# Kernel tuning notes

Hardware: AMD Instinct MI355X
Metric: run time of the kernel (lower is better)

Reference implementation:

```python
import jax, jax.numpy as jnp
import numpy as np

N = 100000  # nodes
NEG_SLOPE = 0.2


def gat_conv(x, W, att_src, att_dst, bias, src, dst):
    # x: [N, Fin], W: [Fin, Fout], att_*: [Fout], bias: [Fout]
    h = x @ W                                    # [N, Fout]
    a_s = h @ att_src                            # [N]
    a_d = h @ att_dst                            # [N]
    e = jax.nn.leaky_relu(a_s[src] + a_d[dst], NEG_SLOPE)  # [E]
    # segment softmax over destination-node neighborhoods
    m = jax.ops.segment_max(e, dst, num_segments=N)        # [N]
    ex = jnp.exp(e - m[dst])
    denom = jax.ops.segment_sum(ex, dst, num_segments=N)   # [N]
    alpha = ex / denom[dst]                      # [E]
    out = jax.ops.segment_sum(alpha[:, None] * h[src], dst, num_segments=N)
    return out + bias


def setup_inputs() -> dict:
    key = jax.random.key(0)
    ks = jax.random.split(key, 10)
    F_in, H, C, E = 512, 16, 40, 3200000
    x = jax.random.normal(ks[0], (N, F_in), dtype=jnp.float32)
    edge_index = jax.random.randint(ks[1], (2, E), 0, N, dtype=jnp.int64)
    s1 = 1.0 / np.sqrt(F_in)
    s2 = 1.0 / np.sqrt(H)
    return {
        "x": x,
        "W1": jax.random.normal(ks[2], (F_in, H), dtype=jnp.float32) * s1,
        "att_src1": jax.random.normal(ks[3], (H,), dtype=jnp.float32) * s2,
        "att_dst1": jax.random.normal(ks[4], (H,), dtype=jnp.float32) * s2,
        "bias1": jnp.zeros((H,), dtype=jnp.float32),
        "W2": jax.random.normal(ks[5], (H, C), dtype=jnp.float32) * s2,
        "att_src2": jax.random.normal(ks[6], (C,), dtype=jnp.float32) / np.sqrt(C),
        "att_dst2": jax.random.normal(ks[7], (C,), dtype=jnp.float32) / np.sqrt(C),
        "bias2": jnp.zeros((C,), dtype=jnp.float32),
        "edge_index": edge_index,
    }


def reference(x, W1, att_src1, att_dst1, bias1, W2, att_src2, att_dst2, bias2, edge_index):
    # add self loops (PyG GATConv default add_self_loops=True)
    loop = jnp.arange(N, dtype=edge_index.dtype)
    src = jnp.concatenate([edge_index[0], loop])
    dst = jnp.concatenate([edge_index[1], loop])
    h = gat_conv(x, W1, att_src1, att_dst1, bias1, src, dst)
    h = jax.nn.relu(h)  # dropout is identity in eval mode
    out = gat_conv(h, W2, att_src2, att_dst2, bias2, src, dst)
    return out
```

## Files before the change

### kernel.cpp

```cpp
#include <hip/hip_runtime.h>
#include <math.h>


constexpr int FIN = 512;
constexpr int F1  = 16;
constexpr int C2  = 40;
constexpr float SLOPE = 0.2f;
constexpr int BSH   = 8;
constexpr int NBMAX = 512;
constexpr int LDSE  = 9728;

__global__ __launch_bounds__(128) void k1_gemm(
    const float* __restrict__ x, const float* __restrict__ W1,
    const float* __restrict__ att_s, const float* __restrict__ att_d,
    float* __restrict__ h1, float* __restrict__ a_s, float* __restrict__ a_d, int n)
{
    __shared__ float WT[F1][FIN + 4];
    for (int idx = threadIdx.x; idx < FIN * F1; idx += 128) {
        int k = idx >> 4, o = idx & 15;
        WT[o][k] = W1[idx];
    }
    __syncthreads();

    const int o0 = (threadIdx.x & 3) * 4;
    const int ng = threadIdx.x >> 2;
    const int node0 = blockIdx.x * 128 + ng * 4;

    const float* xr[4];
#pragma unroll
    for (int nn = 0; nn < 4; ++nn) {
        int node = node0 + nn;
        xr[nn] = x + (size_t)(node < n ? node : 0) * FIN;
    }

    float acc[4][4] = {};
    for (int k = 0; k < FIN; k += 4) {
        float4 wv[4];
#pragma unroll
        for (int oo = 0; oo < 4; ++oo) wv[oo] = *(const float4*)&WT[o0 + oo][k];
#pragma unroll
        for (int nn = 0; nn < 4; ++nn) {
            float4 xv = *(const float4*)(xr[nn] + k);
#pragma unroll
            for (int oo = 0; oo < 4; ++oo)
                acc[nn][oo] += xv.x * wv[oo].x + xv.y * wv[oo].y +
                               xv.z * wv[oo].z + xv.w * wv[oo].w;
        }
    }

#pragma unroll
    for (int nn = 0; nn < 4; ++nn) {
        int node = node0 + nn;
        float ps = 0.f, pd = 0.f;
#pragma unroll
        for (int oo = 0; oo < 4; ++oo) {
            ps += acc[nn][oo] * att_s[o0 + oo];
            pd += acc[nn][oo] * att_d[o0 + oo];
        }
        ps += __shfl_xor(ps, 1); ps += __shfl_xor(ps, 2);
        pd += __shfl_xor(pd, 1); pd += __shfl_xor(pd, 2);
        if (node < n) {
            *(float4*)&h1[(size_t)node * F1 + o0] =
                make_float4(acc[nn][0], acc[nn][1], acc[nn][2], acc[nn][3]);
            if ((threadIdx.x & 3) == 0) { a_s[node] = ps; a_d[node] = pd; }
        }
    }
}

__global__ __launch_bounds__(256) void k_bhist(const int* __restrict__ dst,
                                               int* __restrict__ bcnt, int E, int nb)
{
    __shared__ int cnt[NBMAX];
    for (int t = threadIdx.x; t < NBMAX; t += 256) cnt[t] = 0;
    __syncthreads();
    int base = blockIdx.x * 4096;
#pragma unroll
    for (int k = 0; k < 16; ++k) {
        int e = base + k * 256 + threadIdx.x;
        if (e < E) atomicAdd(&cnt[dst[e] >> BSH], 1);
    }
    __syncthreads();
    for (int t = threadIdx.x; t < nb; t += 256) {
        int c = cnt[t];
        if (c) atomicAdd(&bcnt[t], c);
    }
}

__global__ __launch_bounds__(512) void k_bscan(const int* __restrict__ bcnt,
                                               int* __restrict__ bbase,
                                               int* __restrict__ gcur, int nb, int E)
{
    __shared__ int sc[512];
    int t = threadIdx.x;
    int v = (t < nb) ? bcnt[t] : 0;
    sc[t] = v; __syncthreads();
    for (int off = 1; off < 512; off <<= 1) {
        int u = (t >= off) ? sc[t - off] : 0;
        __syncthreads();
        sc[t] += u;
        __syncthreads();
    }
    int excl = sc[t] - v;
    if (t < nb) { bbase[t] = excl; gcur[t] = excl; }
    if (t == 0) bbase[nb] = E;
}

__global__ __launch_bounds__(256) void k_bucket(const int* __restrict__ src,
                                                const int* __restrict__ dst,
                                                int* __restrict__ gcur,
                                                unsigned int* __restrict__ bpk, int E)
{
    __shared__ int cnt[NBMAX];
    __shared__ int cur[NBMAX];
    for (int t = threadIdx.x; t < NBMAX; t += 256) cnt[t] = 0;
    __syncthreads();
    int base = blockIdx.x * 4096;
#pragma unroll
    for (int k = 0; k < 16; ++k) {
        int e = base + k * 256 + threadIdx.x;
        if (e < E) atomicAdd(&cnt[dst[e] >> BSH], 1);
    }
    __syncthreads();
    for (int t = threadIdx.x; t < NBMAX; t += 256) {
        int c = cnt[t];
        cur[t] = c ? atomicAdd(&gcur[t], c) : 0;
    }
    __syncthreads();
#pragma unroll
    for (int k = 0; k < 16; ++k) {
        int e = base + k * 256 + threadIdx.x;
        if (e < E) {
            int d = dst[e];
            int b = d >> BSH;
            int pos = atomicAdd(&cur[b], 1);
            bpk[pos] = (unsigned)src[e] | ((unsigned)(d & ((1 << BSH) - 1)) << 17);
        }
    }
}

__global__ __launch_bounds__(256) void f1_agg(
    const unsigned int* __restrict__ bpk, const int* __restrict__ bbase,
    const float* __restrict__ h1, const float* __restrict__ a_s, const float* __restrict__ a_d,
    const float* __restrict__ bias1, const float* __restrict__ W2,
    const float* __restrict__ att_s2, const float* __restrict__ att_d2,
    float* __restrict__ hin2, float* __restrict__ pa_s, float* __restrict__ pa_d, int n)
{
    __shared__ int lsrc[LDSE];
    __shared__ int cnt[256];
    __shared__ int scn[256];
    __shared__ float vs[F1], vd[F1], bl[F1];
    const int b = blockIdx.x, t = threadIdx.x;
    const int beg = bbase[b], end = bbase[b + 1];
    const int m = end - beg;

    if (t < 32) {
        int f = t & 15;
        const float* att = (t < 16) ? att_s2 : att_d2;
        float sum = 0.f;
        for (int c = 0; c < C2; ++c) sum += W2[f * C2 + c] * att[c];
        if (t < 16) vs[f] = sum; else vd[f] = sum;
    } else if (t < 48) {
        bl[t - 32] = bias1[t - 32];
    }
    cnt[t] = 0;
    __syncthreads();

    int myBeg = 0, myCnt = 0;
    const bool fits = (m <= LDSE);
    if (fits) {
        for (int j = beg + t; j < end; j += 256)
            atomicAdd(&cnt[(bpk[j] >> 17) & 255], 1);
        __syncthreads();
        int v = cnt[t];
        scn[t] = v;
        __syncthreads();
        for (int off = 1; off < 256; off <<= 1) {
            int u = (t >= off) ? scn[t - off] : 0;
            __syncthreads();
            scn[t] += u;
            __syncthreads();
        }
        myCnt = v;
        myBeg = scn[t] - v;
        cnt[t] = myBeg;
        __syncthreads();
        for (int j = beg + t; j < end; j += 256) {
            unsigned pk = bpk[j];
            int p = atomicAdd(&cnt[(pk >> 17) & 255], 1);
            lsrc[p] = (int)(pk & 0x1FFFFu);
        }
        __syncthreads();
    }

    const int node = (b << BSH) + t;
    if (node >= n) return;

    const float adi = a_d[node];
    float acc[F1];
#pragma unroll
    for (int f = 0; f < F1; ++f) acc[f] = 0.f;
    float den = 0.f;

    if (fits) {
        for (int k = 0; k < myCnt; ++k) {
            int s = lsrc[myBeg + k];
            float ev = a_s[s] + adi;
            ev = (ev >= 0.f) ? ev : SLOPE * ev;
            float ex = __expf(ev);
            den += ex;
            const float4* hp = (const float4*)(h1 + (size_t)s * F1);
#pragma unroll
            for (int q = 0; q < 4; ++q) {
                float4 v = hp[q];
                acc[4*q+0] += ex * v.x; acc[4*q+1] += ex * v.y;
                acc[4*q+2] += ex * v.z; acc[4*q+3] += ex * v.w;
            }
        }
    } else {
        for (int j = beg; j < end; ++j) {
            unsigned pk = bpk[j];
            if ((int)((pk >> 17) & 255) != t) continue;
            int s = (int)(pk & 0x1FFFFu);
            float ev = a_s[s] + adi;
            ev = (ev >= 0.f) ? ev : SLOPE * ev;
            float ex = __expf(ev);
            den += ex;
            const float4* hp = (const float4*)(h1 + (size_t)s * F1);
#pragma unroll
            for (int q = 0; q < 4; ++q) {
                float4 v = hp[q];
                acc[4*q+0] += ex * v.x; acc[4*q+1] += ex * v.y;
                acc[4*q+2] += ex * v.z; acc[4*q+3] += ex * v.w;
            }
        }
    }

    float evs = a_s[node] + adi;
    evs = (evs >= 0.f) ? evs : SLOPE * evs;
    float exs = __expf(evs);
    const float4* hs = (const float4*)(h1 + (size_t)node * F1);
    float inv;
    {
        float d2 = den + exs;
        inv = 1.f / d2;
    }
    float ps = 0.f, pd = 0.f;
    float4* ho = (float4*)(hin2 + (size_t)node * F1);
#pragma unroll
    for (int q = 0; q < 4; ++q) {
        float4 sv = hs[q];
        float4 V;
        V.x = fmaxf((acc[4*q+0] + exs * sv.x) * inv + bl[4*q+0], 0.f);
        V.y = fmaxf((acc[4*q+1] + exs * sv.y) * inv + bl[4*q+1], 0.f);
        V.z = fmaxf((acc[4*q+2] + exs * sv.z) * inv + bl[4*q+2], 0.f);
        V.w = fmaxf((acc[4*q+3] + exs * sv.w) * inv + bl[4*q+3], 0.f);
        ho[q] = V;
        ps += V.x * vs[4*q+0] + V.y * vs[4*q+1] + V.z * vs[4*q+2] + V.w * vs[4*q+3];
        pd += V.x * vd[4*q+0] + V.y * vd[4*q+1] + V.z * vd[4*q+2] + V.w * vd[4*q+3];
    }
    pa_s[node] = ps; pa_d[node] = pd;
}

__global__ __launch_bounds__(256) void f2_agg(
    const unsigned int* __restrict__ bpk, const int* __restrict__ bbase,
    const float* __restrict__ hin2, const float* __restrict__ a_s, const float* __restrict__ a_d,
    const float* __restrict__ W2, const float* __restrict__ bias2,
    float* __restrict__ out, int n)
{
    __shared__ int lsrc[LDSE];
    __shared__ int cnt[256];
    __shared__ int scn[256];
    __shared__ float W2s[F1 * C2];
    __shared__ float b2[C2];
    const int b = blockIdx.x, t = threadIdx.x;
    const int beg = bbase[b], end = bbase[b + 1];
    const int m = end - beg;

    for (int idx = t; idx < F1 * C2; idx += 256) W2s[idx] = W2[idx];
    if (t < C2) b2[t] = bias2[t];
    cnt[t] = 0;
    __syncthreads();

    int myBeg = 0, myCnt = 0;
    const bool fits = (m <= LDSE);
    if (fits) {
        for (int j = beg + t; j < end; j += 256)
            atomicAdd(&cnt[(bpk[j] >> 17) & 255], 1);
        __syncthreads();
        int v = cnt[t];
        scn[t] = v;
        __syncthreads();
        for (int off = 1; off < 256; off <<= 1) {
            int u = (t >= off) ? scn[t - off] : 0;
            __syncthreads();
            scn[t] += u;
            __syncthreads();
        }
        myCnt = v;
        myBeg = scn[t] - v;
        cnt[t] = myBeg;
        __syncthreads();
        for (int j = beg + t; j < end; j += 256) {
            unsigned pk = bpk[j];
            int p = atomicAdd(&cnt[(pk >> 17) & 255], 1);
            lsrc[p] = (int)(pk & 0x1FFFFu);
        }
        __syncthreads();
    }

    const int node = (b << BSH) + t;
    if (node >= n) return;

    const float adi = a_d[node];
    float acc[F1];
#pragma unroll
    for (int f = 0; f < F1; ++f) acc[f] = 0.f;
    float den = 0.f;

    if (fits) {
        for (int k = 0; k < myCnt; ++k) {
            int s = lsrc[myBeg + k];
            float ev = a_s[s] + adi;
            ev = (ev >= 0.f) ? ev : SLOPE * ev;
            float ex = __expf(ev);
            den += ex;
            const float4* hp = (const float4*)(hin2 + (size_t)s * F1);
#pragma unroll
            for (int q = 0; q < 4; ++q) {
                float4 v = hp[q];
                acc[4*q+0] += ex * v.x; acc[4*q+1] += ex * v.y;
                acc[4*q+2] += ex * v.z; acc[4*q+3] += ex * v.w;
            }
        }
    } else {
        for (int j = beg; j < end; ++j) {
            unsigned pk = bpk[j];
            if ((int)((pk >> 17) & 255) != t) continue;
            int s = (int)(pk & 0x1FFFFu);
            float ev = a_s[s] + adi;
            ev = (ev >= 0.f) ? ev : SLOPE * ev;
            float ex = __expf(ev);
            den += ex;
            const float4* hp = (const float4*)(hin2 + (size_t)s * F1);
#pragma unroll
            for (int q = 0; q < 4; ++q) {
                float4 v = hp[q];
                acc[4*q+0] += ex * v.x; acc[4*q+1] += ex * v.y;
                acc[4*q+2] += ex * v.z; acc[4*q+3] += ex * v.w;
            }
        }
    }

    float evs = a_s[node] + adi;
    evs = (evs >= 0.f) ? evs : SLOPE * evs;
    float exs = __expf(evs);
    const float4* hs = (const float4*)(hin2 + (size_t)node * F1);
    float inv = 1.f / (den + exs);
    float val[F1];
#pragma unroll
    for (int q = 0; q < 4; ++q) {
        float4 sv = hs[q];
        val[4*q+0] = (acc[4*q+0] + exs * sv.x) * inv;
        val[4*q+1] = (acc[4*q+1] + exs * sv.y) * inv;
        val[4*q+2] = (acc[4*q+2] + exs * sv.z) * inv;
        val[4*q+3] = (acc[4*q+3] + exs * sv.w) * inv;
    }
    float* op = out + (size_t)node * C2;
    for (int c0 = 0; c0 < C2; c0 += 4) {
        float4 r = make_float4(b2[c0], b2[c0+1], b2[c0+2], b2[c0+3]);
#pragma unroll
        for (int f = 0; f < F1; ++f) {
            float v = val[f];
            r.x += v * W2s[f * C2 + c0 + 0];
            r.y += v * W2s[f * C2 + c0 + 1];
            r.z += v * W2s[f * C2 + c0 + 2];
            r.w += v * W2s[f * C2 + c0 + 3];
        }
        *(float4*)(op + c0) = r;
    }
}

extern "C" void kernel_launch(void* const* d_in, const int* in_sizes, int n_in,
                              void* d_out, int out_size, void* d_ws, size_t ws_size,
                              hipStream_t stream) {
    const float* x      = (const float*)d_in[0];
    const float* W1     = (const float*)d_in[1];
    const float* att_s1 = (const float*)d_in[2];
    const float* att_d1 = (const float*)d_in[3];
    const float* bias1  = (const float*)d_in[4];
    const float* W2     = (const float*)d_in[5];
    const float* att_s2 = (const float*)d_in[6];
    const float* att_d2 = (const float*)d_in[7];
    const float* bias2  = (const float*)d_in[8];
    const int*   edge   = (const int*)d_in[9];

    const int n = in_sizes[0] / FIN;
    const int E = in_sizes[9] / 2;
    const int* src = edge;
    const int* dst = edge + E;
    const int NBK = (n + (1 << BSH) - 1) >> BSH;

    size_t Ns = (size_t)n;
    float* h1    = (float*)d_ws;
    float* hin2  = h1   + 16 * Ns;
    float* a_s1  = hin2 + 16 * Ns;
    float* a_d1  = a_s1 + Ns;
    float* pa_s2 = a_d1 + Ns;
    float* pa_d2 = pa_s2 + Ns;
    int*   bcnt  = (int*)(pa_d2 + Ns);
    int*   bbase = bcnt + NBMAX;
    int*   gcur  = bbase + NBMAX + 1;
    unsigned int* bpk = (unsigned int*)(gcur + NBMAX);
    float* out   = (float*)d_out;

    const int gbA = (E + 4095) / 4096;
    const int gb1 = (n + 127) / 128;

    hipMemsetAsync(bcnt, 0, sizeof(int) * NBMAX, stream);
    k_bhist <<<gbA, 256, 0, stream>>>(dst, bcnt, E, NBK);
    k_bscan <<<1, 512, 0, stream>>>(bcnt, bbase, gcur, NBK, E);
    k_bucket<<<gbA, 256, 0, stream>>>(src, dst, gcur, bpk, E);
    k1_gemm <<<gb1, 128, 0, stream>>>(x, W1, att_s1, att_d1, h1, a_s1, a_d1, n);
    f1_agg  <<<NBK, 256, 0, stream>>>(bpk, bbase, h1, a_s1, a_d1, bias1, W2,
                                      att_s2, att_d2, hin2, pa_s2, pa_d2, n);
    f2_agg  <<<NBK, 256, 0, stream>>>(bpk, bbase, hin2, pa_s2, pa_d2, W2, bias2, out, n);
}
```

Measured before the change: 587.4 us.

## Split aggregation buckets into sub-blocks with four threads per node

Each 256-node destination bucket is now handled by four blocks, each owning 64 nodes, and each node's 16 features are split across four threads that each own one float4. This raises parallelism and occupancy in the aggregation kernels, shrinks per-block LDS to a 3072-entry sub-bucket, and swaps the barrier-heavy 256-wide scan for a 64-lane shuffle scan. The second-layer output projection now goes through shared memory so that four threads share it. The GEMM block size is also doubled to 256. Each sub-block still scans the whole bucket's packed edge list, so bucket reads are repeated four times.

```diff
diff --git a/kernel.cpp b/kernel.cpp
--- a/kernel.cpp
+++ b/kernel.cpp
@@ -8,15 +8,15 @@
 constexpr float SLOPE = 0.2f;
 constexpr int BSH   = 8;
 constexpr int NBMAX = 512;
-constexpr int LDSE  = 9728;
-
-__global__ __launch_bounds__(128) void k1_gemm(
+constexpr int SUBE  = 3072;
+
+__global__ __launch_bounds__(256) void k1_gemm(
     const float* __restrict__ x, const float* __restrict__ W1,
     const float* __restrict__ att_s, const float* __restrict__ att_d,
     float* __restrict__ h1, float* __restrict__ a_s, float* __restrict__ a_d, int n)
 {
     __shared__ float WT[F1][FIN + 4];
-    for (int idx = threadIdx.x; idx < FIN * F1; idx += 128) {
+    for (int idx = threadIdx.x; idx < FIN * F1; idx += 256) {
         int k = idx >> 4, o = idx & 15;
         WT[o][k] = W1[idx];
     }
@@ -24,7 +24,7 @@
 
     const int o0 = (threadIdx.x & 3) * 4;
     const int ng = threadIdx.x >> 2;
-    const int node0 = blockIdx.x * 128 + ng * 4;
+    const int node0 = blockIdx.x * 256 + ng * 4;
 
     const float* xr[4];
 #pragma unroll
@@ -145,13 +145,12 @@
     const float* __restrict__ att_s2, const float* __restrict__ att_d2,
     float* __restrict__ hin2, float* __restrict__ pa_s, float* __restrict__ pa_d, int n)
 {
-    __shared__ int lsrc[LDSE];
-    __shared__ int cnt[256];
-    __shared__ int scn[256];
+    __shared__ int lsrc[SUBE];
+    __shared__ int cnt[64], cur[64], sbeg[64];
     __shared__ float vs[F1], vd[F1], bl[F1];
-    const int b = blockIdx.x, t = threadIdx.x;
+    const int t = threadIdx.x;
+    const int b = blockIdx.x >> 2, sb = blockIdx.x & 3;
     const int beg = bbase[b], end = bbase[b + 1];
-    const int m = end - beg;
 
     if (t < 32) {
         int f = t & 15;
@@ -162,103 +161,90 @@
     } else if (t < 48) {
         bl[t - 32] = bias1[t - 32];
     }
-    cnt[t] = 0;
-    __syncthreads();
-
-    int myBeg = 0, myCnt = 0;
-    const bool fits = (m <= LDSE);
+    if (t < 64) cnt[t] = 0;
+    __syncthreads();
+
+    for (int j = beg + t; j < end; j += 256) {
+        unsigned pk = bpk[j];
+        if (((pk >> 23) & 3u) == (unsigned)sb)
+            atomicAdd(&cnt[(pk >> 17) & 63], 1);
+    }
+    __syncthreads();
+    if (t < 64) {
+        int v = cnt[t], s = v;
+#pragma unroll
+        for (int off = 1; off < 64; off <<= 1) {
+            int u = __shfl_up(s, off);
+            if (t >= off) s += u;
+        }
+        sbeg[t] = s - v;
+        cur[t]  = s - v;
+    }
+    __syncthreads();
+    const int msub = sbeg[63] + cnt[63];
+    const bool fits = (msub <= SUBE);
     if (fits) {
-        for (int j = beg + t; j < end; j += 256)
-            atomicAdd(&cnt[(bpk[j] >> 17) & 255], 1);
-        __syncthreads();
-        int v = cnt[t];
-        scn[t] = v;
-        __syncthreads();
-        for (int off = 1; off < 256; off <<= 1) {
-            int u = (t >= off) ? scn[t - off] : 0;
-            __syncthreads();
-            scn[t] += u;
-            __syncthreads();
-        }
-        myCnt = v;
-        myBeg = scn[t] - v;
-        cnt[t] = myBeg;
-        __syncthreads();
         for (int j = beg + t; j < end; j += 256) {
             unsigned pk = bpk[j];
-            int p = atomicAdd(&cnt[(pk >> 17) & 255], 1);
-            lsrc[p] = (int)(pk & 0x1FFFFu);
-        }
-        __syncthreads();
-    }
-
-    const int node = (b << BSH) + t;
+            if (((pk >> 23) & 3u) == (unsigned)sb) {
+                int p = atomicAdd(&cur[(pk >> 17) & 63], 1);
+                lsrc[p] = (int)(pk & 0x1FFFFu);
+            }
+        }
+    }
+    __syncthreads();
+
+    const int nl = t >> 2, sub = t & 3;
+    const int node = (b << BSH) + (sb << 6) + nl;
     if (node >= n) return;
 
     const float adi = a_d[node];
-    float acc[F1];
-#pragma unroll
-    for (int f = 0; f < F1; ++f) acc[f] = 0.f;
-    float den = 0.f;
+    float a0 = 0.f, a1 = 0.f, a2 = 0.f, a3 = 0.f, den = 0.f;
 
     if (fits) {
-        for (int k = 0; k < myCnt; ++k) {
-            int s = lsrc[myBeg + k];
+        const int mb = sbeg[nl], mc = cnt[nl];
+        const float* hq = h1 + 4 * sub;
+        for (int k = 0; k < mc; ++k) {
+            int s = lsrc[mb + k];
             float ev = a_s[s] + adi;
             ev = (ev >= 0.f) ? ev : SLOPE * ev;
             float ex = __expf(ev);
             den += ex;
-            const float4* hp = (const float4*)(h1 + (size_t)s * F1);
-#pragma unroll
-            for (int q = 0; q < 4; ++q) {
-                float4 v = hp[q];
-                acc[4*q+0] += ex * v.x; acc[4*q+1] += ex * v.y;
-                acc[4*q+2] += ex * v.z; acc[4*q+3] += ex * v.w;
-            }
+            float4 v = *(const float4*)(hq + (size_t)s * F1);
+            a0 += ex * v.x; a1 += ex * v.y; a2 += ex * v.z; a3 += ex * v.w;
         }
     } else {
+        const unsigned key = ((unsigned)sb << 6) | (unsigned)nl;
+        const float* hq = h1 + 4 * sub;
         for (int j = beg; j < end; ++j) {
             unsigned pk = bpk[j];
-            if ((int)((pk >> 17) & 255) != t) continue;
+            if (((pk >> 17) & 255u) != key) continue;
             int s = (int)(pk & 0x1FFFFu);
             float ev = a_s[s] + adi;
             ev = (ev >= 0.f) ? ev : SLOPE * ev;
             float ex = __expf(ev);
             den += ex;
-            const float4* hp = (const float4*)(h1 + (size_t)s * F1);
-#pragma unroll
-            for (int q = 0; q < 4; ++q) {
-                float4 v = hp[q];
-                acc[4*q+0] += ex * v.x; acc[4*q+1] += ex * v.y;
-                acc[4*q+2] += ex * v.z; acc[4*q+3] += ex * v.w;
-            }
+            float4 v = *(const float4*)(hq + (size_t)s * F1);
+            a0 += ex * v.x; a1 += ex * v.y; a2 += ex * v.z; a3 += ex * v.w;
         }
     }
 
     float evs = a_s[node] + adi;
     evs = (evs >= 0.f) ? evs : SLOPE * evs;
     float exs = __expf(evs);
-    const float4* hs = (const float4*)(h1 + (size_t)node * F1);
-    float inv;
-    {
-        float d2 = den + exs;
-        inv = 1.f / d2;
-    }
-    float ps = 0.f, pd = 0.f;
-    float4* ho = (float4*)(hin2 + (size_t)node * F1);
-#pragma unroll
-    for (int q = 0; q < 4; ++q) {
-        float4 sv = hs[q];
-        float4 V;
-        V.x = fmaxf((acc[4*q+0] + exs * sv.x) * inv + bl[4*q+0], 0.f);
-        V.y = fmaxf((acc[4*q+1] + exs * sv.y) * inv + bl[4*q+1], 0.f);
-        V.z = fmaxf((acc[4*q+2] + exs * sv.z) * inv + bl[4*q+2], 0.f);
-        V.w = fmaxf((acc[4*q+3] + exs * sv.w) * inv + bl[4*q+3], 0.f);
-        ho[q] = V;
-        ps += V.x * vs[4*q+0] + V.y * vs[4*q+1] + V.z * vs[4*q+2] + V.w * vs[4*q+3];
-        pd += V.x * vd[4*q+0] + V.y * vd[4*q+1] + V.z * vd[4*q+2] + V.w * vd[4*q+3];
-    }
-    pa_s[node] = ps; pa_d[node] = pd;
+    float inv = 1.f / (den + exs);
+    float4 sv = *(const float4*)(h1 + (size_t)node * F1 + 4 * sub);
+    float4 V;
+    V.x = fmaxf((a0 + exs * sv.x) * inv + bl[4*sub+0], 0.f);
+    V.y = fmaxf((a1 + exs * sv.y) * inv + bl[4*sub+1], 0.f);
+    V.z = fmaxf((a2 + exs * sv.z) * inv + bl[4*sub+2], 0.f);
+    V.w = fmaxf((a3 + exs * sv.w) * inv + bl[4*sub+3], 0.f);
+    *(float4*)(hin2 + (size_t)node * F1 + 4 * sub) = V;
+    float ps = V.x * vs[4*sub+0] + V.y * vs[4*sub+1] + V.z * vs[4*sub+2] + V.w * vs[4*sub+3];
+    float pd = V.x * vd[4*sub+0] + V.y * vd[4*sub+1] + V.z * vd[4*sub+2] + V.w * vd[4*sub+3];
+    ps += __shfl_xor(ps, 1, 4); ps += __shfl_xor(ps, 2, 4);
+    pd += __shfl_xor(pd, 1, 4); pd += __shfl_xor(pd, 2, 4);
+    if (sub == 0) { pa_s[node] = ps; pa_d[node] = pd; }
 }
 
 __global__ __launch_bounds__(256) void f2_agg(
@@ -267,116 +253,102 @@
     const float* __restrict__ W2, const float* __restrict__ bias2,
     float* __restrict__ out, int n)
 {
-    __shared__ int lsrc[LDSE];
-    __shared__ int cnt[256];
-    __shared__ int scn[256];
+    __shared__ int lsrc[SUBE];
+    __shared__ int cnt[64], cur[64], sbeg[64];
     __shared__ float W2s[F1 * C2];
     __shared__ float b2[C2];
-    const int b = blockIdx.x, t = threadIdx.x;
+    __shared__ float vals[64][F1 + 1];
+    const int t = threadIdx.x;
+    const int b = blockIdx.x >> 2, sb = blockIdx.x & 3;
     const int beg = bbase[b], end = bbase[b + 1];
-    const int m = end - beg;
 
     for (int idx = t; idx < F1 * C2; idx += 256) W2s[idx] = W2[idx];
     if (t < C2) b2[t] = bias2[t];
-    cnt[t] = 0;
-    __syncthreads();
-
-    int myBeg = 0, myCnt = 0;
-    const bool fits = (m <= LDSE);
+    if (t < 64) cnt[t] = 0;
+    __syncthreads();
+
+    for (int j = beg + t; j < end; j += 256) {
+        unsigned pk = bpk[j];
+        if (((pk >> 23) & 3u) == (unsigned)sb)
+            atomicAdd(&cnt[(pk >> 17) & 63], 1);
+    }
+    __syncthreads();
+    if (t < 64) {
+        int v = cnt[t], s = v;
+#pragma unroll
+        for (int off = 1; off < 64; off <<= 1) {
+            int u = __shfl_up(s, off);
+            if (t >= off) s += u;
+        }
+        sbeg[t] = s - v;
+        cur[t]  = s - v;
+    }
+    __syncthreads();
+    const int msub = sbeg[63] + cnt[63];
+    const bool fits = (msub <= SUBE);
     if (fits) {
-        for (int j = beg + t; j < end; j += 256)
-            atomicAdd(&cnt[(bpk[j] >> 17) & 255], 1);
-        __syncthreads();
-        int v = cnt[t];
-        scn[t] = v;
-        __syncthreads();
-        for (int off = 1; off < 256; off <<= 1) {
-            int u = (t >= off) ? scn[t - off] : 0;
-            __syncthreads();
-            scn[t] += u;
-            __syncthreads();
-        }
-        myCnt = v;
-        myBeg = scn[t] - v;
-        cnt[t] = myBeg;
-        __syncthreads();
         for (int j = beg + t; j < end; j += 256) {
             unsigned pk = bpk[j];
-            int p = atomicAdd(&cnt[(pk >> 17) & 255], 1);
-            lsrc[p] = (int)(pk & 0x1FFFFu);
-        }
-        __syncthreads();
-    }
-
-    const int node = (b << BSH) + t;
+            if (((pk >> 23) & 3u) == (unsigned)sb) {
+                int p = atomicAdd(&cur[(pk >> 17) & 63], 1);
+                lsrc[p] = (int)(pk & 0x1FFFFu);
+            }
+        }
+    }
+    __syncthreads();
+
+    const int nl = t >> 2, sub = t & 3;
+    const int node = (b << BSH) + (sb << 6) + nl;
     if (node >= n) return;
 
     const float adi = a_d[node];
-    float acc[F1];
-#pragma unroll
-    for (int f = 0; f < F1; ++f) acc[f] = 0.f;
-    float den = 0.f;
+    float a0 = 0.f, a1 = 0.f, a2 = 0.f, a3 = 0.f, den = 0.f;
 
     if (fits) {
-        for (int k = 0; k < myCnt; ++k) {
-            int s = lsrc[myBeg + k];
+        const int mb = sbeg[nl], mc = cnt[nl];
+        const float* hq = hin2 + 4 * sub;
+        for (int k = 0; k < mc; ++k) {
+            int s = lsrc[mb + k];
             float ev = a_s[s] + adi;
             ev = (ev >= 0.f) ? ev : SLOPE * ev;
             float ex = __expf(ev);
             den += ex;
-            const float4* hp = (const float4*)(hin2 + (size_t)s * F1);
-#pragma unroll
-            for (int q = 0; q < 4; ++q) {
-                float4 v = hp[q];
-                acc[4*q+0] += ex * v.x; acc[4*q+1] += ex * v.y;
-                acc[4*q+2] += ex * v.z; acc[4*q+3] += ex * v.w;
-            }
+            float4 v = *(const float4*)(hq + (size_t)s * F1);
+            a0 += ex * v.x; a1 += ex * v.y; a2 += ex * v.z; a3 += ex * v.w;
         }
     } else {
+        const unsigned key = ((unsigned)sb << 6) | (unsigned)nl;
+        const float* hq = hin2 + 4 * sub;
         for (int j = beg; j < end; ++j) {
             unsigned pk = bpk[j];
-            if ((int)((pk >> 17) & 255) != t) continue;
+            if (((pk >> 17) & 255u) != key) continue;
             int s = (int)(pk & 0x1FFFFu);
             float ev = a_s[s] + adi;
             ev = (ev >= 0.f) ? ev : SLOPE * ev;
             float ex = __expf(ev);
             den += ex;
-            const float4* hp = (const float4*)(hin2 + (size_t)s * F1);
-#pragma unroll
-            for (int q = 0; q < 4; ++q) {
-                float4 v = hp[q];
-                acc[4*q+0] += ex * v.x; acc[4*q+1] += ex * v.y;
-                acc[4*q+2] += ex * v.z; acc[4*q+3] += ex * v.w;
-            }
+            float4 v = *(const float4*)(hq + (size_t)s * F1);
+            a0 += ex * v.x; a1 += ex * v.y; a2 += ex * v.z; a3 += ex * v.w;
         }
     }
 
     float evs = a_s[node] + adi;
     evs = (evs >= 0.f) ? evs : SLOPE * evs;
     float exs = __expf(evs);
-    const float4* hs = (const float4*)(hin2 + (size_t)node * F1);
     float inv = 1.f / (den + exs);
-    float val[F1];
-#pragma unroll
-    for (int q = 0; q < 4; ++q) {
-        float4 sv = hs[q];
-        val[4*q+0] = (acc[4*q+0] + exs * sv.x) * inv;
-        val[4*q+1] = (acc[4*q+1] + exs * sv.y) * inv;
-        val[4*q+2] = (acc[4*q+2] + exs * sv.z) * inv;
-        val[4*q+3] = (acc[4*q+3] + exs * sv.w) * inv;
-    }
+    float4 sv = *(const float4*)(hin2 + (size_t)node * F1 + 4 * sub);
+    vals[nl][4*sub+0] = (a0 + exs * sv.x) * inv;
+    vals[nl][4*sub+1] = (a1 + exs * sv.y) * inv;
+    vals[nl][4*sub+2] = (a2 + exs * sv.z) * inv;
+    vals[nl][4*sub+3] = (a3 + exs * sv.w) * inv;
     float* op = out + (size_t)node * C2;
-    for (int c0 = 0; c0 < C2; c0 += 4) {
-        float4 r = make_float4(b2[c0], b2[c0+1], b2[c0+2], b2[c0+3]);
-#pragma unroll
-        for (int f = 0; f < F1; ++f) {
-            float v = val[f];
-            r.x += v * W2s[f * C2 + c0 + 0];
-            r.y += v * W2s[f * C2 + c0 + 1];
-            r.z += v * W2s[f * C2 + c0 + 2];
-            r.w += v * W2s[f * C2 + c0 + 3];
-        }
-        *(float4*)(op + c0) = r;
+#pragma unroll
+    for (int j = 0; j < 10; ++j) {
+        int c = sub + 4 * j;
+        float r = b2[c];
+#pragma unroll
+        for (int f = 0; f < F1; ++f) r += vals[nl][f] * W2s[f * C2 + c];
+        op[c] = r;
     }
 }
 
@@ -414,14 +386,14 @@
     float* out   = (float*)d_out;
 
     const int gbA = (E + 4095) / 4096;
-    const int gb1 = (n + 127) / 128;
+    const int gb1 = (n + 255) / 256;
 
     hipMemsetAsync(bcnt, 0, sizeof(int) * NBMAX, stream);
     k_bhist <<<gbA, 256, 0, stream>>>(dst, bcnt, E, NBK);
     k_bscan <<<1, 512, 0, stream>>>(bcnt, bbase, gcur, NBK, E);
     k_bucket<<<gbA, 256, 0, stream>>>(src, dst, gcur, bpk, E);
-    k1_gemm <<<gb1, 128, 0, stream>>>(x, W1, att_s1, att_d1, h1, a_s1, a_d1, n);
-    f1_agg  <<<NBK, 256, 0, stream>>>(bpk, bbase, h1, a_s1, a_d1, bias1, W2,
-                                      att_s2, att_d2, hin2, pa_s2, pa_d2, n);
-    f2_agg  <<<NBK, 256, 0, stream>>>(bpk, bbase, hin2, pa_s2, pa_d2, W2, bias2, out, n);
-}
+    k1_gemm <<<gb1, 256, 0, stream>>>(x, W1, att_s1, att_d1, h1, a_s1, a_d1, n);
+    f1_agg  <<<NBK * 4, 256, 0, stream>>>(bpk, bbase, h1, a_s1, a_d1, bias1, W2,
+                                          att_s2, att_d2, hin2, pa_s2, pa_d2, n);
+    f2_agg  <<<NBK * 4, 256, 0, stream>>>(bpk, bbase, hin2, pa_s2, pa_d2, W2, bias2, out, n);
+}
```

After: 575.0 us. 1.02x faster.
